# Kernel tuning notes

Hardware: AMD Instinct MI355X
Metric: run time of the kernel (lower is better)

## Reference

```python
import jax, jax.numpy as jnp
import numpy as np
import math

# ---------- real Clebsch-Gordan coupling tables (computed once, tiny) ----------
def _cg(j1, m1, j2, m2, j3, m3):
    if m1 + m2 != m3 or j3 < abs(j1 - j2) or j3 > j1 + j2:
        return 0.0
    f = math.factorial
    pre = ((2 * j3 + 1) * f(j3 + j1 - j2) * f(j3 - j1 + j2) * f(j1 + j2 - j3) / f(j1 + j2 + j3 + 1)) ** 0.5
    pre *= (f(j3 + m3) * f(j3 - m3) * f(j1 - m1) * f(j1 + m1) * f(j2 - m2) * f(j2 + m2)) ** 0.5
    s = 0.0
    for k in range(0, j1 + j2 - j3 + 1):
        d = (k, j1 + j2 - j3 - k, j1 - m1 - k, j2 + m2 - k, j3 - j2 + m1 + k, j3 - j1 - m2 + k)
        if min(d) < 0:
            continue
        den = 1
        for t in d:
            den *= f(t)
        s += (-1) ** k / den
    return pre * s

def _Q(l):  # complex->real spherical-harmonic change of basis
    Q = np.zeros((2 * l + 1, 2 * l + 1), dtype=complex)
    Q[l, l] = 1.0
    s = 2 ** -0.5
    for m in range(1, l + 1):
        Q[l + m, l + m] = (-1) ** m * s
        Q[l + m, l - m] = s
        Q[l - m, l + m] = -1j * (-1) ** m * s
        Q[l - m, l - m] = 1j * s
    return Q

def _K(l1, l2, l3):  # real coupling tensor [2l3+1, 2l1+1, 2l2+1]
    C = np.zeros((2 * l3 + 1, 2 * l1 + 1, 2 * l2 + 1), dtype=complex)
    for M3 in range(-l3, l3 + 1):
        for M1 in range(-l1, l1 + 1):
            for M2 in range(-l2, l2 + 1):
                C[M3 + l3, M1 + l1, M2 + l2] = _cg(l1, M1, l2, M2, l3, M3)
    K = np.einsum('cC,aA,bB,CAB->cab', _Q(l3).conj(), _Q(l1), _Q(l2), C)
    K = K.imag if np.abs(K.imag).max() > np.abs(K.real).max() else K.real
    return np.asarray(K, dtype=np.float32)

# the 9 'uvu' instructions (in_l, edge_l, out_l) with multiplicities (weight_numel=144)
_PATHS = [(0, 0, 0), (0, 2, 2), (1, 0, 1), (1, 2, 1), (1, 2, 2), (2, 0, 2), (2, 2, 0), (2, 2, 1), (2, 2, 2)]
_KT = [jnp.asarray(_K(*p)) for p in _PATHS]
_MULS = [32, 32, 16, 16, 16, 8, 8, 8, 8]
_SPLITS = np.cumsum(_MULS)[:-1].tolist()
NEI = 8
EPS = 1e-5

def _sh(u):  # component-normalized real SH of unit vectors, l=0..2 (m order -l..l, l=1 -> y,z,x)
    x, y, z = u[:, 0], u[:, 1], u[:, 2]
    sh0 = jnp.ones_like(x)[:, None]
    sh1 = np.float32(3 ** 0.5) * jnp.stack([y, z, x], -1)
    s15 = np.float32(15 ** 0.5)
    s5 = np.float32(5 ** 0.5)
    sh2 = jnp.stack([s15 * x * y, s15 * y * z, 0.5 * s5 * (3 * z * z - 1.0), s15 * x * z, 0.5 * s15 * (x * x - y * y)], -1)
    return sh0, sh1, sh2

def _path(xs, sh, wp, Kt):  # xs [E,u,2l1+1], sh [E,2l2+1], Kt [2l3+1,2l1+1,2l2+1] -> [E,u,2l3+1]
    return jnp.einsum('eui,ej,oij->euo', xs, sh, Kt) * wp[None, :, None]

def _layer(x0, x1, x2, pos, src, dst, w, W0, W1, W2, bw0, bb0, bw1, bw2, N):
    ev = pos[dst] - pos[src]
    u = ev / (jnp.linalg.norm(ev, axis=1, keepdims=True) + 1e-12)
    sh0, sh1, sh2 = _sh(u)
    s0 = x0[src][:, :, None]  # [E,32,1]
    s1 = x1[src]              # [E,16,3]
    s2 = x2[src]              # [E,8,5]
    ws = jnp.split(w, _SPLITS)
    p1 = _path(s0, sh0, ws[0], _KT[0])
    p2 = _path(s0, sh2, ws[1], _KT[1])
    p3 = _path(s1, sh0, ws[2], _KT[2])
    p4 = _path(s1, sh2, ws[3], _KT[3])
    p5 = _path(s1, sh2, ws[4], _KT[4])
    p6 = _path(s2, sh0, ws[5], _KT[5])
    p7 = _path(s2, sh2, ws[6], _KT[6])
    p8 = _path(s2, sh2, ws[7], _KT[7])
    p9 = _path(s2, sh2, ws[8], _KT[8])
    m0 = jnp.concatenate([p1, p7], 1)          # [E,40,1]
    m1 = jnp.concatenate([p3, p4, p8], 1)      # [E,40,3]
    m2 = jnp.concatenate([p2, p5, p6, p9], 1)  # [E,64,5]
    a0 = jax.ops.segment_sum(m0, dst, num_segments=N)
    a1 = jax.ops.segment_sum(m1, dst, num_segments=N)
    a2 = jax.ops.segment_sum(m2, dst, num_segments=N)
    y0 = (a0[:, :, 0] @ W0) * np.float32(1.0 / 40 ** 0.5)
    y1 = jnp.einsum('num,uv->nvm', a1, W1) * np.float32(1.0 / 40 ** 0.5)
    y2 = jnp.einsum('num,uv->nvm', a2, W2) * np.float32(1.0 / 64 ** 0.5)
    # equivariant batchnorm (training stats): scalars -> standard BN, l>0 -> norm BN
    f = y0 - y0.mean(0)
    y0 = f / jnp.sqrt((f * f).mean(0) + EPS) * bw0 + bb0
    y1 = y1 / jnp.sqrt((y1 * y1).mean(axis=(0, 2)) + EPS)[None, :, None] * bw1[None, :, None]
    y2 = y2 / jnp.sqrt((y2 * y2).mean(axis=(0, 2)) + EPS)[None, :, None] * bw2[None, :, None]
    return y0, y1, y2

def _forward(positions, W_emb, tp_w, lin_W0, lin_W1, lin_W2, bn_w0, bn_b0, bn_w1, bn_w2, Wf1, Wf2, bf2, Wf3, bf3):
    B, P, _ = positions.shape
    N = B * P
    pos = positions.reshape(N, 3)
    # kNN graph from dense cdist + topk (indices are not differentiated)
    pg = jax.lax.stop_gradient(pos)
    sq = jnp.sum(pg * pg, 1)
    d2 = sq[:, None] + sq[None, :] - 2.0 * (pg @ pg.T)
    _, idx = jax.lax.top_k(-d2, NEI + 1)  # smallest distances; col 0 is self
    src = jnp.repeat(jnp.arange(N), NEI)
    dst = idx[:, 1:].reshape(-1)
    x0 = jnp.ones((N, 1), jnp.float32) @ W_emb  # embedding: only 0e->0e path exists
    x1 = jnp.zeros((N, 16, 3), jnp.float32)
    x2 = jnp.zeros((N, 8, 5), jnp.float32)
    for l in range(3):
        y0, y1, y2 = _layer(x0, x1, x2, pos, src, dst, tp_w[l], lin_W0[l], lin_W1[l], lin_W2[l],
                            bn_w0[l], bn_b0[l], bn_w1[l], bn_w2[l], N)
        x0 = jax.nn.relu(y0) + x0
        x1 = jax.nn.relu(y1) + x1
        x2 = jax.nn.relu(y2) + x2
    h = jax.nn.relu((x0 @ Wf1) * np.float32(1.0 / 32 ** 0.5))  # scalar part -> 32x0e
    h = jax.nn.relu(h @ Wf2 + bf2)
    out = (h @ Wf3 + bf3).reshape(B, P, 2)
    return out

def setup_inputs() -> dict:
    key = jax.random.key(0)
    ks = jax.random.split(key, 16)
    B, P = 4, 2048
    return {
        'positions': jax.random.normal(ks[0], (B, P, 3), jnp.float32) * 3.0,
        'W_emb': jax.random.normal(ks[1], (1, 32), jnp.float32),
        'tp_w': jax.random.normal(ks[2], (3, 144), jnp.float32),
        'lin_W0': jax.random.normal(ks[3], (3, 40, 32), jnp.float32),
        'lin_W1': jax.random.normal(ks[4], (3, 40, 16), jnp.float32),
        'lin_W2': jax.random.normal(ks[5], (3, 64, 8), jnp.float32),
        'bn_w0': 1.0 + 0.05 * jax.random.normal(ks[6], (3, 32), jnp.float32),
        'bn_b0': jnp.zeros((3, 32), jnp.float32),
        'bn_w1': 1.0 + 0.05 * jax.random.normal(ks[7], (3, 16), jnp.float32),
        'bn_w2': 1.0 + 0.05 * jax.random.normal(ks[8], (3, 8), jnp.float32),
        'Wf1': jax.random.normal(ks[9], (32, 32), jnp.float32),
        'Wf2': jax.random.normal(ks[10], (32, 16), jnp.float32) * 0.2,
        'bf2': jax.random.normal(ks[11], (16,), jnp.float32) * 0.1,
        'Wf3': jax.random.normal(ks[12], (16, 2), jnp.float32) * 0.2,
        'bf3': jax.random.normal(ks[13], (2,), jnp.float32) * 0.1,
    }

def reference(positions, W_emb, tp_w, lin_W0, lin_W1, lin_W2, bn_w0, bn_b0, bn_w1, bn_w2, Wf1, Wf2, bf2, Wf3, bf3):
    return _forward(positions, W_emb, tp_w, lin_W0, lin_W1, lin_W2, bn_w0, bn_b0, bn_w1, bn_w2, Wf1, Wf2, bf2, Wf3, bf3)
```

## Files before the change

kernel.cpp:

```cpp
#include <hip/hip_runtime.h>
#include <math.h>

#define NN 8192
#define REV_CAP 48
#define KNN_CAP 384
#define PF 12

static const size_t OFF_K     = 0;
static const size_t OFF_CNT   = 512;
static const size_t OFF_REV   = 8704;
static const size_t OFF_STATS = 401920;
static const size_t OFF_XF    = 406528;
static const size_t OFF_YF    = 1389568;
static const size_t WS_FLOATS = 2372608;

static double h_dfact(int n){ double r=1.0; for(int i=2;i<=n;++i) r*=(double)i; return r; }

static double h_dcg(int j1,int m1,int j2,int m2,int j3,int m3){
  if (m1+m2!=m3) return 0.0;
  if (j3 < abs(j1-j2) || j3 > j1+j2) return 0.0;
  double pre = sqrt((double)(2*j3+1)*h_dfact(j3+j1-j2)*h_dfact(j3-j1+j2)*h_dfact(j1+j2-j3)/h_dfact(j1+j2+j3+1));
  pre *= sqrt(h_dfact(j3+m3)*h_dfact(j3-m3)*h_dfact(j1-m1)*h_dfact(j1+m1)*h_dfact(j2-m2)*h_dfact(j2+m2));
  double s=0.0;
  for(int k=0;k<=j1+j2-j3;++k){
    int d1=j1+j2-j3-k, d2=j1-m1-k, d3=j2+m2-k, d4=j3-j2+m1+k, d5=j3-j1-m2+k;
    if(d1<0||d2<0||d3<0||d4<0||d5<0) continue;
    double den = h_dfact(k)*h_dfact(d1)*h_dfact(d2)*h_dfact(d3)*h_dfact(d4)*h_dfact(d5);
    s += ((k&1)? -1.0: 1.0)/den;
  }
  return pre*s;
}

static int h_qrow(int l,int r,int* col,double* re,double* im){
  const double s = 0.70710678118654752440;
  if (r==l){ col[0]=l; re[0]=1.0; im[0]=0.0; return 1; }
  if (r>l){ int m=r-l;
    col[0]=l+m; re[0]=((m&1)?-s:s); im[0]=0.0;
    col[1]=l-m; re[1]=s;            im[1]=0.0;
  } else { int m=l-r;
    col[0]=l+m; re[0]=0.0; im[0]=((m&1)? s : -s);
    col[1]=l-m; re[1]=0.0; im[1]=s;
  }
  return 2;
}

static float g_Khost[405];
static bool  g_Kinit = false;

static void h_computeK(){
  const int sizes[9]={1,25,9,45,75,25,25,75,125};
  const int l1s[9]={0,0,1,1,1,2,2,2,2};
  const int l2s[9]={0,2,0,2,2,0,2,2,2};
  const int l3s[9]={0,2,1,1,2,2,0,1,2};
  for(int tid=0; tid<405; ++tid){
    int p=0, rem=tid;
    for(p=0;p<9;++p){ if(rem < sizes[p]) break; rem -= sizes[p]; }
    const int l1=l1s[p], l2=l2s[p], l3=l3s[p];
    const int n1=2*l1+1, n2=2*l2+1;
    const int c = rem/(n1*n2); const int r2 = rem%(n1*n2); const int a=r2/n2; const int b=r2%n2;

    int c3[2],c1[2],c2[2]; double re3[2],im3[2],re1[2],im1[2],re2[2],im2[2];
    const int nc3 = h_qrow(l3,c,c3,re3,im3);
    const int nc1 = h_qrow(l1,a,c1,re1,im1);
    const int nc2 = h_qrow(l2,b,c2,re2,im2);

    double accRe=0, accIm=0;
    for(int i3=0;i3<nc3;++i3){
      const double q3re=re3[i3], q3im=-im3[i3];
      for(int i1=0;i1<nc1;++i1){
        const double pre_re = q3re*re1[i1] - q3im*im1[i1];
        const double pre_im = q3re*im1[i1] + q3im*re1[i1];
        for(int i2=0;i2<nc2;++i2){
          const double cgv = h_dcg(l1, c1[i1]-l1, l2, c2[i2]-l2, l3, c3[i3]-l3);
          if (cgv==0.0) continue;
          accRe += (pre_re*re2[i2] - pre_im*im2[i2])*cgv;
          accIm += (pre_re*im2[i2] + pre_im*re2[i2])*cgv;
        }
      }
    }
    const bool useImag = ((l1+l2+l3)&1)!=0;
    g_Khost[tid] = (float)(useImag? accIm : accRe);
  }
}

__global__ __launch_bounds__(256) void k_setup(const float* __restrict__ pos,
        const float* __restrict__ W_emb,
        float* __restrict__ xf,
        float* __restrict__ xs, float* __restrict__ ys, float* __restrict__ zs,
        float* __restrict__ qs,
        int* __restrict__ cnt, float* __restrict__ stats){
  int idx = blockIdx.x*256 + threadIdx.x;
  if (idx < 983040) { const int c = idx%120; xf[idx] = (c<32)? W_emb[c] : 0.f; return; }
  idx -= 983040;
  if (idx < 8192) {
    const float x=pos[3*idx], y=pos[3*idx+1], z=pos[3*idx+2];
    xs[idx]=x; ys[idx]=y; zs[idx]=z; qs[idx]=0.5f*(x*x+y*y+z*z);
    return;
  }
  idx -= 8192;
  if (idx < 8192) { cnt[idx]=0; return; }
  idx -= 8192;
  if (idx < 3072) stats[idx]=0.f;
}

__device__ __forceinline__ unsigned fkey(float f){
  const unsigned b = __float_as_uint(f);
  return (b & 0x80000000u) ? ~b : (b | 0x80000000u);
}

__device__ __forceinline__ float rsel9_T(float m1, float m2){
  const unsigned kk1 = fkey(m1), kk2 = fkey(m2);
  unsigned P = 0u; int need = 9;
  #pragma unroll 1
  for(int bit=31; bit>=0; --bit){
    const unsigned pref = P >> bit;
    const int c0 = __popcll(__ballot((kk1>>bit)==pref)) + __popcll(__ballot((kk2>>bit)==pref));
    if (need > c0){ need -= c0; P |= (1u<<bit); }
  }
  return __uint_as_float((P & 0x80000000u) ? (P & 0x7fffffffu) : ~P);
}

#define RSELECT_PUSH(KMAX) do{ \
  unsigned P = 0u; int need = 9; \
  _Pragma("unroll 1") \
  for(int bit=31; bit>=0; --bit){ \
    const unsigned pref = P >> bit; \
    int c0 = 0; \
    _Pragma("unroll") \
    for(int k=0;k<KMAX;++k) c0 += __popcll(__ballot((ku[k]>>bit)==pref)); \
    if (need > c0){ need -= c0; P |= (1u<<bit); } \
  } \
  int c_eq = 0; \
  _Pragma("unroll") \
  for(int k=0;k<KMAX;++k) c_eq += __popcll(__ballot(ku[k]==P)); \
  bool tsel[KMAX]; \
  _Pragma("unroll") \
  for(int k=0;k<KMAX;++k) tsel[k] = (ku[k]==P); \
  if (c_eq > need){ \
    _Pragma("unroll") \
    for(int k=0;k<KMAX;++k) tsel[k]=false; \
    for(int r=0;r<need;++r){ \
      int mid = 0x7fffffff; \
      _Pragma("unroll") \
      for(int k=0;k<KMAX;++k) if (ku[k]==P && !tsel[k] && il[k]<mid) mid = il[k]; \
      _Pragma("unroll") \
      for(int s=32;s>0;s>>=1){ const int om = __shfl_xor(mid,s,64); mid = (om<mid)? om : mid; } \
      _Pragma("unroll") \
      for(int k=0;k<KMAX;++k) if (ku[k]==P && il[k]==mid) tsel[k]=true; \
    } \
  } \
  _Pragma("unroll") \
  for(int k=0;k<KMAX;++k){ \
    const bool take = (ku[k] < P) || tsel[k]; \
    const int ix = il[k]; \
    if (take && ix != node){ \
      int cpos = atomicAdd(&cnt[ix],1); \
      if (cpos < REV_CAP) rev[ix*REV_CAP + cpos] = node; \
    } \
  } \
}while(0)

__global__ __launch_bounds__(256, 8) void k_knn8(const float* __restrict__ xs,
                                              const float* __restrict__ ys,
                                              const float* __restrict__ zs,
                                              const float* __restrict__ qs,
                                              int* __restrict__ cnt, int* __restrict__ rev){
  const int lane = threadIdx.x & 63;
  const int w    = threadIdx.x >> 6;
  const int n0   = blockIdx.x*8 + w*2;
  const int w2   = w*2;
  __shared__ float sdist[8][KNN_CAP];
  __shared__ int   sidx[8][KNN_CAP];
  __shared__ int   scount[8];
  if (threadIdx.x < 8) scount[threadIdx.x]=0;
  __syncthreads();

  const float px0 = xs[n0],   py0 = ys[n0],   pz0 = zs[n0];
  const float px1 = xs[n0+1], py1 = ys[n0+1], pz1 = zs[n0+1];

  float m1a=INFINITY, m2a=INFINITY, m1b=INFINITY, m2b=INFINITY;
  for(int c=0;c<4;++c){
    const int base = (c*64 + lane)*4;
    const float4 fx = *(const float4*)(xs + base);
    const float4 fy = *(const float4*)(ys + base);
    const float4 fz = *(const float4*)(zs + base);
    const float4 fq = *(const float4*)(qs + base);
    const float cx[4]={fx.x,fx.y,fx.z,fx.w};
    const float cy[4]={fy.x,fy.y,fy.z,fy.w};
    const float cz[4]={fz.x,fz.y,fz.z,fz.w};
    const float cq[4]={fq.x,fq.y,fq.z,fq.w};
    #pragma unroll
    for(int q=0;q<4;++q){
      const float s0 = fmaf(-px0,cx[q], fmaf(-py0,cy[q], fmaf(-pz0,cz[q], cq[q])));
      const float s1 = fmaf(-px1,cx[q], fmaf(-py1,cy[q], fmaf(-pz1,cz[q], cq[q])));
      float hi;
      hi = fmaxf(m1a, s0); m1a = fminf(m1a, s0); m2a = fminf(m2a, hi);
      hi = fmaxf(m1b, s1); m1b = fminf(m1b, s1); m2b = fminf(m2b, hi);
    }
  }
  const float T0 = rsel9_T(m1a, m2a);
  const float T1 = rsel9_T(m1b, m2b);

  {
    const int b0 = lane*4;
    float4 nfx = *(const float4*)(xs + b0);
    float4 nfy = *(const float4*)(ys + b0);
    float4 nfz = *(const float4*)(zs + b0);
    float4 nfq = *(const float4*)(qs + b0);
    for(int c=0;c<32;++c){
      const float4 fx=nfx, fy=nfy, fz=nfz, fq=nfq;
      const int cbase = (c*64 + lane)*4;
      if (c<31){
        const int nb2 = ((c+1)*64 + lane)*4;
        nfx = *(const float4*)(xs + nb2);
        nfy = *(const float4*)(ys + nb2);
        nfz = *(const float4*)(zs + nb2);
        nfq = *(const float4*)(qs + nb2);
      }
      const float cx[4]={fx.x,fx.y,fx.z,fx.w};
      const float cy[4]={fy.x,fy.y,fy.z,fy.w};
      const float cz[4]={fz.x,fz.y,fz.z,fz.w};
      const float cq[4]={fq.x,fq.y,fq.z,fq.w};
      #pragma unroll
      for(int q=0;q<4;++q){
        const float s0 = fmaf(-px0,cx[q], fmaf(-py0,cy[q], fmaf(-pz0,cz[q], cq[q])));
        const float s1 = fmaf(-px1,cx[q], fmaf(-py1,cy[q], fmaf(-pz1,cz[q], cq[q])));
        if (s0 <= T0){
          int pos = atomicAdd(&scount[w2],1);
          if (pos < KNN_CAP){ sdist[w2][pos]=s0; sidx[w2][pos]=cbase+q; }
        }
        if (s1 <= T1){
          int pos = atomicAdd(&scount[w2+1],1);
          if (pos < KNN_CAP){ sdist[w2+1][pos]=s1; sidx[w2+1][pos]=cbase+q; }
        }
      }
    }
  }
  __syncthreads();

  #pragma unroll 1
  for(int u=0;u<2;++u){
    const int node = n0+u;
    const int s_   = w2+u;
    int m = scount[s_]; if (m > KNN_CAP) m = KNN_CAP;
    unsigned ku[KNN_CAP/64]; int il[KNN_CAP/64];
    #pragma unroll
    for(int k=0;k<KNN_CAP/64;++k){
      const int j = lane + 64*k;
      if (j < m){ ku[k]=fkey(sdist[s_][j]); il[k]=sidx[s_][j]; }
      else      { ku[k]=0xffffffffu;        il[k]=0x7fffffff; }
    }
    if (m <= 128) RSELECT_PUSH(2);
    else          RSELECT_PUSH(6);
  }
}

__global__ __launch_bounds__(256) void k_msg(
  const float* __restrict__ pos,
  const int* __restrict__ cnt, const int* __restrict__ rev,
  const float* __restrict__ Kbuf,
  const float* __restrict__ xf,
  const float* __restrict__ tpw,
  const float* __restrict__ W0, const float* __restrict__ W1, const float* __restrict__ W2,
  float* __restrict__ pA, float* __restrict__ pB,
  float* __restrict__ yf)
{
  const int t = threadIdx.x;
  const int w = t >> 6;
  const int lane = t & 63;
  const int n = blockIdx.x*4 + w;

  __shared__ float KL[405];
  __shared__ float TW[144];
  __shared__ float momPS[4][720];
  __shared__ float aS[4][480];
  __shared__ int   eIdx[4][REV_CAP];
  __shared__ float eSh[4][5][REV_CAP];
  __shared__ float bA[32], bB[96];
  for(int q=t;q<405;q+=256) KL[q]=Kbuf[q];
  for(int q=t;q<144;q+=256) TW[q]=tpw[q];
  if (t<96){ bB[t]=0.f; if(t<32) bA[t]=0.f; }

  const int deg0 = cnt[n];
  const int deg = (deg0<REV_CAP)? deg0 : REV_CAP;
  const float pnx=pos[3*n], pny=pos[3*n+1], pnz=pos[3*n+2];
  const float s15 = 3.8729833462f, s5c = 2.2360679775f;
  if (lane < deg){
    const int i = rev[n*REV_CAP+lane];
    eIdx[w][lane] = i;
    const float ex = pnx - pos[3*i], ey = pny - pos[3*i+1], ez = pnz - pos[3*i+2];
    const float rn = sqrtf(ex*ex+ey*ey+ez*ez) + 1e-12f;
    const float ux=ex/rn, uy=ey/rn, uz=ez/rn;
    eSh[w][0][lane]=s15*ux*uy;
    eSh[w][1][lane]=s15*uy*uz;
    eSh[w][2][lane]=0.5f*s5c*(3.f*uz*uz-1.f);
    eSh[w][3][lane]=s15*ux*uz;
    eSh[w][4][lane]=0.5f*s15*(ux*ux-uy*uy);
  }
  __syncthreads();

  const int c0 = lane*2;
  float mp0=0.f, mp1=0.f;
  float ms0[5], ms1[5];
  #pragma unroll
  for(int j=0;j<5;++j){ ms0[j]=0.f; ms1[j]=0.f; }

  int idxr[PF];
  #pragma unroll
  for(int k=0;k<PF;++k) idxr[k] = (k<deg)? eIdx[w][k] : 0;
  float2 fr[PF];
  if (lane<60){
    #pragma unroll
    for(int k=0;k<PF;++k) fr[k] = *(const float2*)(xf + (size_t)idxr[k]*120 + c0);
  }
  #pragma unroll
  for(int k=0;k<PF;++k){
    if (k<deg){
      const float sh0=eSh[w][0][k], sh1=eSh[w][1][k], sh2=eSh[w][2][k];
      const float sh3=eSh[w][3][k], sh4=eSh[w][4][k];
      if (lane<60){
        const float2 f = fr[k];
        mp0 += f.x; mp1 += f.y;
        ms0[0]+=f.x*sh0; ms0[1]+=f.x*sh1; ms0[2]+=f.x*sh2; ms0[3]+=f.x*sh3; ms0[4]+=f.x*sh4;
        ms1[0]+=f.y*sh0; ms1[1]+=f.y*sh1; ms1[2]+=f.y*sh2; ms1[3]+=f.y*sh3; ms1[4]+=f.y*sh4;
      }
    }
  }
  for(int e=PF;e<deg;++e){
    const int i = eIdx[w][e];
    const float sh0=eSh[w][0][e], sh1=eSh[w][1][e], sh2=eSh[w][2][e];
    const float sh3=eSh[w][3][e], sh4=eSh[w][4][e];
    if (lane<60){
      const float2 f = *(const float2*)(xf + (size_t)i*120 + c0);
      mp0 += f.x; mp1 += f.y;
      ms0[0]+=f.x*sh0; ms0[1]+=f.x*sh1; ms0[2]+=f.x*sh2; ms0[3]+=f.x*sh3; ms0[4]+=f.x*sh4;
      ms1[0]+=f.y*sh0; ms1[1]+=f.y*sh1; ms1[2]+=f.y*sh2; ms1[3]+=f.y*sh3; ms1[4]+=f.y*sh4;
    }
  }
  if (lane<60){
    momPS[w][c0]=mp0; momPS[w][c0+1]=mp1;
    #pragma unroll
    for(int j=0;j<5;++j){ momPS[w][120+c0*5+j]=ms0[j]; momPS[w][120+(c0+1)*5+j]=ms1[j]; }
  }
  __syncthreads();

  #pragma unroll 1
  for(int e=lane; e<480; e+=64){
    int a, b, L, dst; float rw;
    if (e<32){        const int u=e;                            a=0;        b=u;                  L=1;  rw=TW[u];     dst=u; }
    else if (e<192){  const int i=e-32,  u=i/5, o=i%5;          a=1+o*5;    b=120+u*5;            L=5;  rw=TW[32+u];  dst=160+u*5+o; }
    else if (e<240){  const int i=e-192, u=i/3, o=i%3;          a=26+o*3;   b=32+u*3;             L=3;  rw=TW[64+u];  dst=40+u*3+o; }
    else if (e<288){  const int i=e-240, u=i/3, o=i%3;          a=35+o*15;  b=120+(32+u*3)*5;     L=15; rw=TW[80+u];  dst=40+(16+u)*3+o; }
    else if (e<368){  const int i=e-288, u=i/5, o=i%5;          a=80+o*15;  b=120+(32+u*3)*5;     L=15; rw=TW[96+u];  dst=160+(32+u)*5+o; }
    else if (e<408){  const int i=e-368, u=i/5, o=i%5;          a=155+o*5;  b=80+u*5;             L=5;  rw=TW[112+u]; dst=160+(48+u)*5+o; }
    else if (e<416){  const int u=e-408;                        a=180;      b=120+(80+u*5)*5;     L=25; rw=TW[120+u]; dst=32+u; }
    else if (e<440){  const int i=e-416, u=i/3, o=i%3;          a=205+o*25; b=120+(80+u*5)*5;     L=25; rw=TW[128+u]; dst=40+(32+u)*3+o; }
    else {            const int i=e-440, u=i/5, o=i%5;          a=280+o*25; b=120+(80+u*5)*5;     L=25; rw=TW[136+u]; dst=160+(56+u)*5+o; }
    float g=0.f;
    #pragma unroll 1
    for(int k=0;k<L;++k) g += KL[a+k]*momPS[w][b+k];
    aS[w][dst] = rw*g;
  }
  __syncthreads();

  const float inv40 = 0.15811388300841896660f;
  for(int q=lane;q<120;q+=64){
    float out; int chan;
    if (q<32){
      float g=0.f;
      for(int uu=0;uu<40;++uu) g += aS[w][uu]*W0[uu*32+q];
      out = g*inv40; chan = q;
    } else if (q<80){
      const int e=q-32, v=e/3, m=e%3;
      float g=0.f;
      for(int uu=0;uu<40;++uu) g += aS[w][40+uu*3+m]*W1[uu*16+v];
      out = g*inv40; chan = 32+v;
    } else {
      const int e=q-80, tt=e/5, m=e%5;
      float g=0.f;
      for(int uu=0;uu<64;++uu) g += aS[w][160+uu*5+m]*W2[uu*8+tt];
      out = g*0.125f; chan = 48+tt;
    }
    yf[(size_t)n*120+q] = out;
    atomicAdd(&bB[chan], out*out);
    if (q<32) atomicAdd(&bA[q], out);
  }
  __syncthreads();
  if (t<96){
    const int slot = blockIdx.x & 7;
    atomicAdd(&pB[slot*96 + t], bB[t]);
    if (t<32) atomicAdd(&pA[slot*32 + t], bA[t]);
  }
}

__global__ __launch_bounds__(256) void k_norm(const float* __restrict__ yf,
                       const float* __restrict__ pA, const float* __restrict__ pB,
                       const float* __restrict__ bw0,const float* __restrict__ bb0,
                       const float* __restrict__ bw1,const float* __restrict__ bw2,
                       float* __restrict__ xf){
  __shared__ float sc[96], sf[32];
  const int t = threadIdx.x;
  if (t<96){
    float sB=0.f;
    #pragma unroll
    for(int k=0;k<8;++k) sB += pB[k*96+t];
    float scale;
    if (t<32){
      float sA=0.f;
      #pragma unroll
      for(int k=0;k<8;++k) sA += pA[k*32+t];
      const float mean = sA*(1.f/8192.f);
      const float var  = sB*(1.f/8192.f) - mean*mean;
      const float inv  = 1.f/sqrtf(var+1e-5f);
      scale = bw0[t]*inv;
      sf[t] = bb0[t] - mean*scale;
    } else if (t<48){
      scale = bw1[t-32]/sqrtf(sB*(1.f/(8192.f*3.f))+1e-5f);
    } else {
      scale = bw2[t-48]/sqrtf(sB*(1.f/(8192.f*5.f))+1e-5f);
    }
    sc[t]=scale;
  }
  __syncthreads();
  const int idx = blockIdx.x*256 + t;
  if (idx >= NN*120) return;
  const int c = idx%120;
  const int chan = (c<32)? c : ((c<80)? 32+(c-32)/3 : 48+(c-80)/5);
  const float v = yf[idx]*sc[chan] + ((c<32)? sf[c] : 0.f);
  xf[idx] += fmaxf(v,0.f);
}

__global__ __launch_bounds__(256) void k_normmlp(const float* __restrict__ yf,
                                             const float* __restrict__ xf,
                                             const float* __restrict__ pA, const float* __restrict__ pB,
                                             const float* __restrict__ bw0,const float* __restrict__ bb0,
                                             const float* __restrict__ Wf1,const float* __restrict__ Wf2,
                                             const float* __restrict__ bf2,const float* __restrict__ Wf3,
                                             const float* __restrict__ bf3, float* __restrict__ out){
  __shared__ float w1[1024], w2[512], w3[32], b2[16], b3[2], sc0[32], sf0[32];
  __shared__ float xvS[4][32], h1S[4][32], h2S[4][16];
  const int t=threadIdx.x;
  const int w = t>>6, lane = t&63;
  const int n = blockIdx.x*4 + w;
  for(int q=t;q<1024;q+=256) w1[q]=Wf1[q];
  for(int q=t;q<512;q+=256)  w2[q]=Wf2[q];
  if(t<32) w3[t]=Wf3[t];
  if(t<16) b2[t]=bf2[t];
  if(t<2)  b3[t]=bf3[t];
  if(t<32){
    float sA=0.f, sB=0.f;
    #pragma unroll
    for(int k=0;k<8;++k){ sA += pA[k*32+t]; sB += pB[k*96+t]; }
    const float mean = sA*(1.f/8192.f);
    const float var  = sB*(1.f/8192.f) - mean*mean;
    const float inv  = 1.f/sqrtf(var+1e-5f);
    sc0[t] = bw0[t]*inv;
    sf0[t] = bb0[t] - mean*sc0[t];
  }
  __syncthreads();
  if (lane<32){
    const float v = yf[(size_t)n*120+lane]*sc0[lane] + sf0[lane];
    xvS[w][lane] = xf[(size_t)n*120+lane] + fmaxf(v,0.f);
  }
  __syncthreads();
  const float inv32 = 0.17677669529663688110f;
  if (lane<32){
    float g=0.f;
    #pragma unroll 8
    for(int k=0;k<32;++k) g += xvS[w][k]*w1[k*32+lane];
    h1S[w][lane] = fmaxf(g*inv32, 0.f);
  }
  __syncthreads();
  if (lane<16){
    float g=b2[lane];
    #pragma unroll 8
    for(int k=0;k<32;++k) g += h1S[w][k]*w2[k*16+lane];
    h2S[w][lane]=fmaxf(g,0.f);
  }
  __syncthreads();
  if (lane<2){
    float g=b3[lane];
    #pragma unroll
    for(int k=0;k<16;++k) g += h2S[w][k]*w3[k*2+lane];
    out[n*2+lane]=g;
  }
}

extern "C" void kernel_launch(void* const* d_in, const int* in_sizes, int n_in,
                              void* d_out, int out_size, void* d_ws, size_t ws_size,
                              hipStream_t stream) {
  const float* positions = (const float*)d_in[0];
  const float* W_emb  = (const float*)d_in[1];
  const float* tp_w   = (const float*)d_in[2];
  const float* lin_W0 = (const float*)d_in[3];
  const float* lin_W1 = (const float*)d_in[4];
  const float* lin_W2 = (const float*)d_in[5];
  const float* bn_w0  = (const float*)d_in[6];
  const float* bn_b0  = (const float*)d_in[7];
  const float* bn_w1  = (const float*)d_in[8];
  const float* bn_w2  = (const float*)d_in[9];
  const float* Wf1 = (const float*)d_in[10];
  const float* Wf2 = (const float*)d_in[11];
  const float* bf2 = (const float*)d_in[12];
  const float* Wf3 = (const float*)d_in[13];
  const float* bf3 = (const float*)d_in[14];

  if (ws_size < WS_FLOATS*sizeof(float)) return;

  float* ws    = (float*)d_ws;
  float* Kbuf  = ws + OFF_K;
  int*   cnt   = (int*)(ws + OFF_CNT);
  int*   rev   = (int*)(ws + OFF_REV);
  float* stats = ws + OFF_STATS;
  float* xf = ws + OFF_XF;
  float* yf = ws + OFF_YF;

  float* xs = yf;
  float* ysA = yf + NN;
  float* zs = yf + 2*NN;
  float* qs = yf + 3*NN;

  if (!g_Kinit){ h_computeK(); g_Kinit = true; }
  hipMemcpyAsync(Kbuf, g_Khost, 405*sizeof(float), hipMemcpyHostToDevice, stream);

  k_setup<<<3916,256,0,stream>>>(positions, W_emb, xf, xs, ysA, zs, qs, cnt, stats);
  k_knn8<<<NN/8,256,0,stream>>>(xs, ysA, zs, qs, cnt, rev);

  for(int l=0;l<3;++l){
    float* pA = stats + l*1024;
    float* pB = pA + 256;
    k_msg<<<NN/4,256,0,stream>>>(positions, cnt, rev, Kbuf, xf,
                              tp_w + l*144, lin_W0 + l*40*32, lin_W1 + l*40*16, lin_W2 + l*64*8,
                              pA, pB, yf);
    if (l<2){
      k_norm<<<(NN*120+255)/256,256,0,stream>>>(yf, pA, pB,
                              bn_w0 + l*32, bn_b0 + l*32, bn_w1 + l*16, bn_w2 + l*8,
                              xf);
    }
  }
  k_normmlp<<<NN/4,256,0,stream>>>(yf, xf, stats + 2*1024, stats + 2*1024 + 256,
                              bn_w0 + 64, bn_b0 + 64,
                              Wf1, Wf2, bf2, Wf3, bf3, (float*)d_out);
}
```

Measured before the change: 268.5 us.

## Fuse per-layer message, norm and MLP kernels into one cooperative persistent kernel

Replaces the per-layer sequence of k_msg/k_norm launches and the final k_normmlp with a single cooperative kernel over a fixed grid of 1536 blocks. Blocks loop over node groups and use grid-wide syncs between phases, which removes several kernel launches and their drain gaps. The fallback path keeps the old launches if the cooperative launch fails. The cost is grid.sync overhead and reduced parallelism from the persistent grid, plus possible lower occupancy from the launch bounds.

Result: slower. 275.7 us (+2.7%).

```diff
diff --git a/kernel.cpp b/kernel.cpp
--- a/kernel.cpp
+++ b/kernel.cpp
@@ -1,10 +1,14 @@
 #include <hip/hip_runtime.h>
+#include <hip/hip_cooperative_groups.h>
 #include <math.h>
+
+namespace cg = cooperative_groups;
 
 #define NN 8192
 #define REV_CAP 48
 #define KNN_CAP 384
 #define PF 12
+#define LGRID 1536
 
 static const size_t OFF_K     = 0;
 static const size_t OFF_CNT   = 512;
@@ -46,6 +50,7 @@
 
 static float g_Khost[405];
 static bool  g_Kinit = false;
+static int   g_coop  = -1;
 
 static void h_computeK(){
   const int sizes[9]={1,25,9,45,75,25,25,75,125};
@@ -255,30 +260,24 @@
   }
 }
 
-__global__ __launch_bounds__(256) void k_msg(
-  const float* __restrict__ pos,
-  const int* __restrict__ cnt, const int* __restrict__ rev,
-  const float* __restrict__ Kbuf,
+
+__device__ __forceinline__ void msg_group_body(
+  float* __restrict__ smem, int t, int w, int lane, int grp,
+  const float* __restrict__ pos, const int* __restrict__ cnt, const int* __restrict__ rev,
   const float* __restrict__ xf,
-  const float* __restrict__ tpw,
   const float* __restrict__ W0, const float* __restrict__ W1, const float* __restrict__ W2,
-  float* __restrict__ pA, float* __restrict__ pB,
-  float* __restrict__ yf)
+  float* __restrict__ pA, float* __restrict__ pB, float* __restrict__ yf)
 {
-  const int t = threadIdx.x;
-  const int w = t >> 6;
-  const int lane = t & 63;
-  const int n = blockIdx.x*4 + w;
-
-  __shared__ float KL[405];
-  __shared__ float TW[144];
-  __shared__ float momPS[4][720];
-  __shared__ float aS[4][480];
-  __shared__ int   eIdx[4][REV_CAP];
-  __shared__ float eSh[4][5][REV_CAP];
-  __shared__ float bA[32], bB[96];
-  for(int q=t;q<405;q+=256) KL[q]=Kbuf[q];
-  for(int q=t;q<144;q+=256) TW[q]=tpw[q];
+  float* KL    = smem;
+  float* TW    = smem + 405;
+  float* momPS = smem + 549;
+  float* aS    = smem + 3429;
+  float* bA    = smem + 5349;
+  float* bB    = smem + 5381;
+  int*   eIdx  = (int*)(smem + 5477);
+  float* eSh   = smem + 5669;
+  const int n = grp*4 + w;
+
   if (t<96){ bB[t]=0.f; if(t<32) bA[t]=0.f; }
 
   const int deg0 = cnt[n];
@@ -287,15 +286,15 @@
   const float s15 = 3.8729833462f, s5c = 2.2360679775f;
   if (lane < deg){
     const int i = rev[n*REV_CAP+lane];
-    eIdx[w][lane] = i;
+    eIdx[w*48+lane] = i;
     const float ex = pnx - pos[3*i], ey = pny - pos[3*i+1], ez = pnz - pos[3*i+2];
     const float rn = sqrtf(ex*ex+ey*ey+ez*ez) + 1e-12f;
     const float ux=ex/rn, uy=ey/rn, uz=ez/rn;
-    eSh[w][0][lane]=s15*ux*uy;
-    eSh[w][1][lane]=s15*uy*uz;
-    eSh[w][2][lane]=0.5f*s5c*(3.f*uz*uz-1.f);
-    eSh[w][3][lane]=s15*ux*uz;
-    eSh[w][4][lane]=0.5f*s15*(ux*ux-uy*uy);
+    eSh[(w*5+0)*48+lane]=s15*ux*uy;
+    eSh[(w*5+1)*48+lane]=s15*uy*uz;
+    eSh[(w*5+2)*48+lane]=0.5f*s5c*(3.f*uz*uz-1.f);
+    eSh[(w*5+3)*48+lane]=s15*ux*uz;
+    eSh[(w*5+4)*48+lane]=0.5f*s15*(ux*ux-uy*uy);
   }
   __syncthreads();
 
@@ -307,7 +306,7 @@
 
   int idxr[PF];
   #pragma unroll
-  for(int k=0;k<PF;++k) idxr[k] = (k<deg)? eIdx[w][k] : 0;
+  for(int k=0;k<PF;++k) idxr[k] = (k<deg)? eIdx[w*48+k] : 0;
   float2 fr[PF];
   if (lane<60){
     #pragma unroll
@@ -316,8 +315,8 @@
   #pragma unroll
   for(int k=0;k<PF;++k){
     if (k<deg){
-      const float sh0=eSh[w][0][k], sh1=eSh[w][1][k], sh2=eSh[w][2][k];
-      const float sh3=eSh[w][3][k], sh4=eSh[w][4][k];
+      const float sh0=eSh[(w*5+0)*48+k], sh1=eSh[(w*5+1)*48+k], sh2=eSh[(w*5+2)*48+k];
+      const float sh3=eSh[(w*5+3)*48+k], sh4=eSh[(w*5+4)*48+k];
       if (lane<60){
         const float2 f = fr[k];
         mp0 += f.x; mp1 += f.y;
@@ -327,9 +326,9 @@
     }
   }
   for(int e=PF;e<deg;++e){
-    const int i = eIdx[w][e];
-    const float sh0=eSh[w][0][e], sh1=eSh[w][1][e], sh2=eSh[w][2][e];
-    const float sh3=eSh[w][3][e], sh4=eSh[w][4][e];
+    const int i = eIdx[w*48+e];
+    const float sh0=eSh[(w*5+0)*48+e], sh1=eSh[(w*5+1)*48+e], sh2=eSh[(w*5+2)*48+e];
+    const float sh3=eSh[(w*5+3)*48+e], sh4=eSh[(w*5+4)*48+e];
     if (lane<60){
       const float2 f = *(const float2*)(xf + (size_t)i*120 + c0);
       mp0 += f.x; mp1 += f.y;
@@ -338,9 +337,9 @@
     }
   }
   if (lane<60){
-    momPS[w][c0]=mp0; momPS[w][c0+1]=mp1;
+    momPS[w*720+c0]=mp0; momPS[w*720+c0+1]=mp1;
     #pragma unroll
-    for(int j=0;j<5;++j){ momPS[w][120+c0*5+j]=ms0[j]; momPS[w][120+(c0+1)*5+j]=ms1[j]; }
+    for(int j=0;j<5;++j){ momPS[w*720+120+c0*5+j]=ms0[j]; momPS[w*720+120+(c0+1)*5+j]=ms1[j]; }
   }
   __syncthreads();
 
@@ -358,8 +357,8 @@
     else {            const int i=e-440, u=i/5, o=i%5;          a=280+o*25; b=120+(80+u*5)*5;     L=25; rw=TW[136+u]; dst=160+(56+u)*5+o; }
     float g=0.f;
     #pragma unroll 1
-    for(int k=0;k<L;++k) g += KL[a+k]*momPS[w][b+k];
-    aS[w][dst] = rw*g;
+    for(int k=0;k<L;++k) g += KL[a+k]*momPS[w*720+b+k];
+    aS[w*480+dst] = rw*g;
   }
   __syncthreads();
 
@@ -368,17 +367,17 @@
     float out; int chan;
     if (q<32){
       float g=0.f;
-      for(int uu=0;uu<40;++uu) g += aS[w][uu]*W0[uu*32+q];
+      for(int uu=0;uu<40;++uu) g += aS[w*480+uu]*W0[uu*32+q];
       out = g*inv40; chan = q;
     } else if (q<80){
       const int e=q-32, v=e/3, m=e%3;
       float g=0.f;
-      for(int uu=0;uu<40;++uu) g += aS[w][40+uu*3+m]*W1[uu*16+v];
+      for(int uu=0;uu<40;++uu) g += aS[w*480+40+uu*3+m]*W1[uu*16+v];
       out = g*inv40; chan = 32+v;
     } else {
       const int e=q-80, tt=e/5, m=e%5;
       float g=0.f;
-      for(int uu=0;uu<64;++uu) g += aS[w][160+uu*5+m]*W2[uu*8+tt];
+      for(int uu=0;uu<64;++uu) g += aS[w*480+160+uu*5+m]*W2[uu*8+tt];
       out = g*0.125f; chan = 48+tt;
     }
     yf[(size_t)n*120+q] = out;
@@ -387,10 +386,157 @@
   }
   __syncthreads();
   if (t<96){
-    const int slot = blockIdx.x & 7;
+    const int slot = grp & 7;
     atomicAdd(&pB[slot*96 + t], bB[t]);
     if (t<32) atomicAdd(&pA[slot*32 + t], bA[t]);
   }
+  __syncthreads();
+}
+
+__global__ __launch_bounds__(256, 6) void k_layers(
+  const float* __restrict__ pos,
+  const int* __restrict__ cnt, const int* __restrict__ rev,
+  const float* __restrict__ Kbuf,
+  float* __restrict__ xf,
+  const float* __restrict__ tp_w,
+  const float* __restrict__ lin_W0, const float* __restrict__ lin_W1, const float* __restrict__ lin_W2,
+  float* __restrict__ stats,
+  float* __restrict__ yf,
+  const float* __restrict__ bn_w0, const float* __restrict__ bn_b0,
+  const float* __restrict__ bn_w1, const float* __restrict__ bn_w2,
+  const float* __restrict__ Wf1, const float* __restrict__ Wf2,
+  const float* __restrict__ bf2, const float* __restrict__ Wf3,
+  const float* __restrict__ bf3, float* __restrict__ out)
+{
+  cg::grid_group grid = cg::this_grid();
+  __shared__ float smem[6629];
+  const int t = threadIdx.x;
+  const int w = t>>6, lane = t&63;
+
+  for (int l=0; l<3; ++l){
+    const float* tpw = tp_w + l*144;
+    const float* W0  = lin_W0 + l*1280;
+    const float* W1  = lin_W1 + l*640;
+    const float* W2  = lin_W2 + l*512;
+    float* pA = stats + l*1024;
+    float* pB = pA + 256;
+
+    for(int q=t;q<405;q+=256) smem[q]=Kbuf[q];
+    for(int q=t;q<144;q+=256) smem[405+q]=tpw[q];
+    __syncthreads();
+    for (int grp = blockIdx.x; grp < NN/4; grp += gridDim.x)
+      msg_group_body(smem, t, w, lane, grp, pos, cnt, rev, xf, W0, W1, W2, pA, pB, yf);
+    grid.sync();
+
+    if (l < 2){
+      float* sc = smem; float* sf = smem + 96;
+      const float* bw0 = bn_w0 + l*32; const float* bb0 = bn_b0 + l*32;
+      const float* bw1 = bn_w1 + l*16; const float* bw2 = bn_w2 + l*8;
+      if (t<96){
+        float sB=0.f;
+        #pragma unroll
+        for(int k=0;k<8;++k) sB += pB[k*96+t];
+        float scale;
+        if (t<32){
+          float sA=0.f;
+          #pragma unroll
+          for(int k=0;k<8;++k) sA += pA[k*32+t];
+          const float mean = sA*(1.f/8192.f);
+          const float var  = sB*(1.f/8192.f) - mean*mean;
+          const float inv  = 1.f/sqrtf(var+1e-5f);
+          scale = bw0[t]*inv;
+          sf[t] = bb0[t] - mean*scale;
+        } else if (t<48){
+          scale = bw1[t-32]/sqrtf(sB*(1.f/(8192.f*3.f))+1e-5f);
+        } else {
+          scale = bw2[t-48]/sqrtf(sB*(1.f/(8192.f*5.f))+1e-5f);
+        }
+        sc[t]=scale;
+      }
+      __syncthreads();
+      for (int chunk = blockIdx.x; chunk < (NN*120)/256; chunk += gridDim.x){
+        const int idx = chunk*256 + t;
+        const int c = idx%120;
+        const int chan = (c<32)? c : ((c<80)? 32+(c-32)/3 : 48+(c-80)/5);
+        const float v = yf[idx]*sc[chan] + ((c<32)? sf[c] : 0.f);
+        xf[idx] += fmaxf(v,0.f);
+      }
+      grid.sync();
+    }
+  }
+
+  {
+    float* w1 = smem;          float* w2 = smem+1024;  float* w3 = smem+1536;
+    float* b2 = smem+1568;     float* b3 = smem+1584;
+    float* sc0 = smem+1586;    float* sf0 = smem+1618;
+    float* xvS = smem+1650;    float* h1S = smem+1778; float* h2S = smem+1906;
+    const float* pA2 = stats + 2*1024; const float* pB2 = pA2 + 256;
+    for(int q=t;q<1024;q+=256) w1[q]=Wf1[q];
+    for(int q=t;q<512;q+=256)  w2[q]=Wf2[q];
+    if(t<32) w3[t]=Wf3[t];
+    if(t<16) b2[t]=bf2[t];
+    if(t<2)  b3[t]=bf3[t];
+    if(t<32){
+      float sA=0.f, sB=0.f;
+      #pragma unroll
+      for(int k=0;k<8;++k){ sA += pA2[k*32+t]; sB += pB2[k*96+t]; }
+      const float mean = sA*(1.f/8192.f);
+      const float var  = sB*(1.f/8192.f) - mean*mean;
+      const float inv  = 1.f/sqrtf(var+1e-5f);
+      sc0[t] = (bn_w0+64)[t]*inv;
+      sf0[t] = (bn_b0+64)[t] - mean*sc0[t];
+    }
+    __syncthreads();
+    const float inv32 = 0.17677669529663688110f;
+    for (int grp = blockIdx.x; grp < NN/4; grp += gridDim.x){
+      const int n = grp*4 + w;
+      if (lane<32){
+        const float v = yf[(size_t)n*120+lane]*sc0[lane] + sf0[lane];
+        xvS[w*32+lane] = xf[(size_t)n*120+lane] + fmaxf(v,0.f);
+      }
+      __syncthreads();
+      if (lane<32){
+        float g=0.f;
+        #pragma unroll 8
+        for(int k=0;k<32;++k) g += xvS[w*32+k]*w1[k*32+lane];
+        h1S[w*32+lane] = fmaxf(g*inv32, 0.f);
+      }
+      __syncthreads();
+      if (lane<16){
+        float g=b2[lane];
+        #pragma unroll 8
+        for(int k=0;k<32;++k) g += h1S[w*32+k]*w2[k*16+lane];
+        h2S[w*16+lane]=fmaxf(g,0.f);
+      }
+      __syncthreads();
+      if (lane<2){
+        float g=b3[lane];
+        #pragma unroll
+        for(int k=0;k<16;++k) g += h2S[w*16+k]*w3[k*2+lane];
+        out[n*2+lane]=g;
+      }
+      __syncthreads();
+    }
+  }
+}
+
+__global__ __launch_bounds__(256) void k_msg(
+  const float* __restrict__ pos,
+  const int* __restrict__ cnt, const int* __restrict__ rev,
+  const float* __restrict__ Kbuf,
+  const float* __restrict__ xf,
+  const float* __restrict__ tpw,
+  const float* __restrict__ W0, const float* __restrict__ W1, const float* __restrict__ W2,
+  float* __restrict__ pA, float* __restrict__ pB,
+  float* __restrict__ yf)
+{
+  __shared__ float smem[6629];
+  const int t = threadIdx.x;
+  const int w = t>>6, lane = t&63;
+  for(int q=t;q<405;q+=256) smem[q]=Kbuf[q];
+  for(int q=t;q<144;q+=256) smem[405+q]=tpw[q];
+  __syncthreads();
+  msg_group_body(smem, t, w, lane, blockIdx.x, pos, cnt, rev, xf, W0, W1, W2, pA, pB, yf);
 }
 
 __global__ __launch_bounds__(256) void k_norm(const float* __restrict__ yf,
@@ -526,6 +672,20 @@
   k_setup<<<3916,256,0,stream>>>(positions, W_emb, xf, xs, ysA, zs, qs, cnt, stats);
   k_knn8<<<NN/8,256,0,stream>>>(xs, ysA, zs, qs, cnt, rev);
 
+  if (g_coop != 0){
+    float* outp = (float*)d_out;
+    void* args[] = { (void*)&positions, (void*)&cnt, (void*)&rev, (void*)&Kbuf,
+                     (void*)&xf, (void*)&tp_w, (void*)&lin_W0, (void*)&lin_W1, (void*)&lin_W2,
+                     (void*)&stats, (void*)&yf, (void*)&bn_w0, (void*)&bn_b0,
+                     (void*)&bn_w1, (void*)&bn_w2, (void*)&Wf1, (void*)&Wf2,
+                     (void*)&bf2, (void*)&Wf3, (void*)&bf3, (void*)&outp };
+    hipError_t e = hipLaunchCooperativeKernel((const void*)k_layers,
+                     dim3(LGRID), dim3(256), args, 0, stream);
+    if (e == hipSuccess){ g_coop = 1; return; }
+    (void)hipGetLastError();
+    g_coop = 0;
+  }
+
   for(int l=0;l<3;++l){
     float* pA = stats + l*1024;
     float* pB = pA + 256;
```
